# Optimization experiments

Measured on AMD Instinct MI355X. Metric: run time of the kernel, lower is better.

The kernel has to match this reference:

```python
import jax, jax.numpy as jnp
import numpy as np

D_MODEL = 1024
N_HEADS = 16
HEAD_DIM = D_MODEL // N_HEADS


def setup_inputs() -> dict:
    key = jax.random.key(0)
    ks = jax.random.split(key, 10)
    B, NQ, S = 8, 64, 4096
    inv = 1.0 / np.sqrt(D_MODEL)
    inp = {
        "queries": jax.random.normal(ks[0], (B, NQ, D_MODEL), dtype=jnp.float32),
        "context": jax.random.normal(ks[1], (B, S, D_MODEL), dtype=jnp.float32),
        "wq": jax.random.normal(ks[2], (D_MODEL, D_MODEL), dtype=jnp.float32) * inv,
        "bq": jnp.zeros((D_MODEL,), dtype=jnp.float32),
        "wk": jax.random.normal(ks[3], (D_MODEL, D_MODEL), dtype=jnp.float32) * inv,
        "bk": jnp.zeros((D_MODEL,), dtype=jnp.float32),
        "wv": jax.random.normal(ks[4], (D_MODEL, D_MODEL), dtype=jnp.float32) * inv,
        "bv": jnp.zeros((D_MODEL,), dtype=jnp.float32),
        "wo": jax.random.normal(ks[5], (D_MODEL, D_MODEL), dtype=jnp.float32) * inv,
        "bo": jnp.zeros((D_MODEL,), dtype=jnp.float32),
    }
    return inp


def reference(queries, context, wq, bq, wk, bk, wv, bv, wo, bo):
    B, NQ, D = queries.shape
    S = context.shape[1]
    H, HD = N_HEADS, HEAD_DIM
    scale = HD ** -0.5
    # projections (x @ W^T + b, matching nn.Linear)
    q = queries @ wq.T + bq            # (B, NQ, D)
    k = context @ wk.T + bk            # (B, S, D)
    v = context @ wv.T + bv            # (B, S, D)
    q = q.reshape(B, NQ, H, HD).transpose(0, 2, 1, 3)  # (B, H, NQ, HD)
    k = k.reshape(B, S, H, HD).transpose(0, 2, 1, 3)   # (B, H, S, HD)
    v = v.reshape(B, S, H, HD).transpose(0, 2, 1, 3)   # (B, H, S, HD)
    attn = jnp.einsum('bhnd,bhsd->bhns', q, k) * scale
    attn = jax.nn.softmax(attn, axis=-1)
    # dropout is identity at eval / p=0
    out = jnp.einsum('bhns,bhsd->bhnd', attn, v)        # (B, H, NQ, HD)
    out = out.transpose(0, 2, 1, 3).reshape(B, NQ, D)   # (B, NQ, D)
    return out @ wo.T + bo
```

## Files before the change

### kernel.cpp

```cpp
#include <hip/hip_runtime.h>
#include <stdint.h>

#define BATCH   8
#define NQL     64
#define SLEN    4096
#define DMODEL  1024
#define NHEADS  16
#define HDIM    64

typedef float          f32x4  __attribute__((ext_vector_type(4)));
typedef float          f32x16 __attribute__((ext_vector_type(16)));
typedef __bf16         bf16x8 __attribute__((ext_vector_type(8)));
typedef unsigned int   u32x4  __attribute__((ext_vector_type(4)));
typedef unsigned short u16x4  __attribute__((ext_vector_type(4)));
typedef unsigned short u16x8  __attribute__((ext_vector_type(8)));

__device__ __forceinline__ unsigned short f2bf(float f) {
  unsigned int u = __builtin_bit_cast(unsigned int, f);
  u += 0x7FFFu + ((u >> 16) & 1u);
  return (unsigned short)(u >> 16);
}

__device__ __forceinline__ f32x4 mfma16(bf16x8 a, bf16x8 b, f32x4 c) {
  return __builtin_amdgcn_mfma_f32_16x16x32_bf16(a, b, c, 0, 0, 0);
}

__device__ __forceinline__ bf16x8 lds_frag(const char* p) {
  u32x4 v = *(const u32x4*)p;
  return __builtin_bit_cast(bf16x8, v);
}

__device__ __forceinline__ void gload_lds16(const void* g, void* l) {
  __builtin_amdgcn_global_load_lds((const __attribute__((address_space(1))) void*)g,
                                   (__attribute__((address_space(3))) void*)l, 16, 0, 0);
}

__global__ __launch_bounds__(256) void cvt_bf16_kernel(const float* __restrict__ in,
                                                       unsigned short* __restrict__ out,
                                                       int n8) {
  int i = blockIdx.x * 256 + threadIdx.x;
  if (i >= n8) return;
  const float4* p = (const float4*)in + (size_t)i * 2;
  float4 a = p[0], b = p[1];
  u16x8 o;
  o[0] = f2bf(a.x); o[1] = f2bf(a.y); o[2] = f2bf(a.z); o[3] = f2bf(a.w);
  o[4] = f2bf(b.x); o[5] = f2bf(b.y); o[6] = f2bf(b.z); o[7] = f2bf(b.w);
  *((u16x8*)out + i) = o;
}

#define GF(a) ((a) ^ (((((a) >> 7) & 3) << 4) | ((((a) >> 9) & 1) << 6)))

template<int MODE>
__global__ __launch_bounds__(512, 2)
void gemm256(const unsigned short* __restrict__ A, const unsigned short* __restrict__ Bw,
             const float* __restrict__ bias, void* __restrict__ Cout,
             int M, int N, int K) {
  __shared__ char lds[98304];

  const int tid = threadIdx.x;
  const int wid = tid >> 6, lane = tid & 63;
  const int l31 = lane & 31, lhi = lane >> 5;
  const int wm = wid >> 2, wn = wid & 3;

  const int nbn = N >> 8;
  const int cpx = (int)gridDim.x >> 3;
  const int bid = (int)blockIdx.x;
  const int wg  = (bid & 7) * cpx + (bid >> 3);
  const int brow = (wg / nbn) << 8;
  const int bcol = (wg % nbn) << 8;

  const int dA0 = wid * 1024 + lane * 16;
  const int dA1 = dA0 + 8192;
  const int a0 = GF(dA0), a1 = GF(dA1);
  const int r0s = a0 >> 6, g0 = (a0 >> 4) & 3;
  const int r1s = a1 >> 6, g1 = (a1 >> 4) & 3;
  const unsigned short* srcA0 = A + (size_t)(brow + r0s) * K + g0 * 8;
  const unsigned short* srcA1 = A + (size_t)(brow + r1s) * K + g1 * 8;
  const unsigned short* srcB0 = Bw + (size_t)(bcol + r0s) * K + g0 * 8;
  const unsigned short* srcB1 = Bw + (size_t)(bcol + r1s) * K + g1 * 8;
  const int db0 = wid * 1024;
  const int db1 = db0 + 8192;

  int offA[4][2], offB[2][2];
#pragma unroll
  for (int mi = 0; mi < 4; ++mi)
#pragma unroll
    for (int ks = 0; ks < 2; ++ks) {
      int r = wm * 128 + mi * 32 + l31;
      int a = r * 64 + ks * 32 + lhi * 16;
      offA[mi][ks] = GF(a);
    }
#pragma unroll
  for (int ni = 0; ni < 2; ++ni)
#pragma unroll
    for (int ks = 0; ks < 2; ++ks) {
      int r = wn * 64 + ni * 32 + l31;
      int a = r * 64 + ks * 32 + lhi * 16;
      offB[ni][ks] = GF(a) + 16384;
    }

  f32x16 acc[4][2];
#pragma unroll
  for (int mi = 0; mi < 4; ++mi)
#pragma unroll
    for (int ni = 0; ni < 2; ++ni)
#pragma unroll
      for (int e = 0; e < 16; ++e) acc[mi][ni][e] = 0.f;

  auto stage = [&](int kt, int bo) {
    const int ko = kt << 5;
    char* base = lds + bo;
    gload_lds16(srcA0 + ko, base + db0);
    gload_lds16(srcA1 + ko, base + db1);
    gload_lds16(srcB0 + ko, base + 16384 + db0);
    gload_lds16(srcB1 + ko, base + 16384 + db1);
  };

  const int KT = K >> 5;
  stage(0, 0);
  stage(1, 32768);
  asm volatile("s_waitcnt vmcnt(4)" ::: "memory");
  __builtin_amdgcn_s_barrier();
  __builtin_amdgcn_sched_barrier(0);

  int bo = 0;
  for (int kt = 0; kt < KT; ++kt) {
    const bool st = (kt + 2 < KT);
    if (st) {
      int bo2 = bo + 65536;
      if (bo2 >= 98304) bo2 -= 98304;
      stage(kt + 2, bo2);
    }
    const char* bA = lds + bo;
    bf16x8 af[4][2], bfr[2][2];
#pragma unroll
    for (int mi = 0; mi < 4; ++mi)
#pragma unroll
      for (int ks = 0; ks < 2; ++ks) af[mi][ks] = lds_frag(bA + offA[mi][ks]);
#pragma unroll
    for (int ni = 0; ni < 2; ++ni)
#pragma unroll
      for (int ks = 0; ks < 2; ++ks) bfr[ni][ks] = lds_frag(bA + offB[ni][ks]);

    __builtin_amdgcn_s_setprio(1);
#pragma unroll
    for (int ks = 0; ks < 2; ++ks)
#pragma unroll
      for (int mi = 0; mi < 4; ++mi)
#pragma unroll
        for (int ni = 0; ni < 2; ++ni)
          acc[mi][ni] = __builtin_amdgcn_mfma_f32_32x32x16_bf16(af[mi][ks], bfr[ni][ks],
                                                                acc[mi][ni], 0, 0, 0);
    __builtin_amdgcn_s_setprio(0);

    if (kt + 1 < KT) {
      if (st) asm volatile("s_waitcnt vmcnt(4)" ::: "memory");
      else    asm volatile("s_waitcnt vmcnt(0)" ::: "memory");
      __builtin_amdgcn_s_barrier();
      __builtin_amdgcn_sched_barrier(0);
    }
    bo = (bo == 65536) ? 0 : bo + 32768;
  }

#pragma unroll
  for (int mi = 0; mi < 4; ++mi) {
#pragma unroll
    for (int ni = 0; ni < 2; ++ni) {
      f32x16 v = acc[mi][ni];
      const int c = bcol + wn * 64 + ni * 32 + l31;
      const float bi = bias[c];
      const int rbase = brow + wm * 128 + mi * 32 + lhi * 4;
      if constexpr (MODE == 0) {
        unsigned short* Cb = (unsigned short*)Cout;
#pragma unroll
        for (int q = 0; q < 4; ++q)
#pragma unroll
          for (int j = 0; j < 4; ++j)
            Cb[(size_t)(rbase + q * 8 + j) * N + c] = f2bf(v[q * 4 + j] + bi);
      } else {
        unsigned short* Vt = (unsigned short*)Cout;
        const size_t fb = ((size_t)(rbase >> 12) * 1024 + c) * 4096;
#pragma unroll
        for (int q = 0; q < 4; ++q) {
          u16x4 pk;
#pragma unroll
          for (int j = 0; j < 4; ++j) pk[j] = f2bf(v[q * 4 + j] + bi);
          *(u16x4*)(Vt + fb + ((rbase + q * 8) & 4095)) = pk;
        }
      }
    }
  }
}

template<int MODE>
__global__ __launch_bounds__(256)
void gemm_bt(const unsigned short* __restrict__ A, const unsigned short* __restrict__ Bw,
             const float* __restrict__ bias, void* __restrict__ Cout,
             int M, int N, int K) {
  __shared__ char lds[32768];
  char* ldsA = lds;
  char* ldsB = lds + 16384;

  const int tid  = threadIdx.x;
  const int wave = tid >> 6, lane = tid & 63;
  const int g    = lane >> 4, ln = lane & 15;
  const int nbn  = N >> 7;
  const int brow = (int)(blockIdx.x / nbn) << 7;
  const int bcol = (int)(blockIdx.x % nbn) << 7;
  const int wr   = wave >> 1, wc = wave & 1;

  f32x4 acc[4][4];
#pragma unroll
  for (int i = 0; i < 4; ++i)
#pragma unroll
    for (int j = 0; j < 4; ++j) acc[i][j] = (f32x4){0.f, 0.f, 0.f, 0.f};

  const int KT = K >> 6;
  const int srow = lane >> 3;
  const int srcs = (lane & 7) ^ (srow & 7);

  for (int kt = 0; kt < KT; ++kt) {
#pragma unroll
    for (int c = wave; c < 16; c += 4) {
      int row = (c << 3) + srow;
      const char* ga = (const char*)A + (((size_t)(brow + row) * K + (kt << 6) + (srcs << 3)) << 1);
      gload_lds16(ga, ldsA + (c << 10));
      const char* gb = (const char*)Bw + (((size_t)(bcol + row) * K + (kt << 6) + (srcs << 3)) << 1);
      gload_lds16(gb, ldsB + (c << 10));
    }
    asm volatile("s_waitcnt vmcnt(0)" ::: "memory");
    __syncthreads();

#pragma unroll
    for (int ks = 0; ks < 2; ++ks) {
      bf16x8 af[4], bfr[4];
      const int slot = ((ks << 2) + g) ^ (ln & 7);
#pragma unroll
      for (int mt = 0; mt < 4; ++mt) {
        int row = wr * 64 + mt * 16 + ln;
        af[mt] = lds_frag(ldsA + row * 128 + (slot << 4));
      }
#pragma unroll
      for (int nt = 0; nt < 4; ++nt) {
        int row = wc * 64 + nt * 16 + ln;
        bfr[nt] = lds_frag(ldsB + row * 128 + (slot << 4));
      }
      __builtin_amdgcn_s_setprio(1);
#pragma unroll
      for (int mt = 0; mt < 4; ++mt)
#pragma unroll
        for (int nt = 0; nt < 4; ++nt)
          acc[mt][nt] = mfma16(af[mt], bfr[nt], acc[mt][nt]);
      __builtin_amdgcn_s_setprio(0);
    }
    __syncthreads();
  }

#pragma unroll
  for (int mt = 0; mt < 4; ++mt) {
#pragma unroll
    for (int nt = 0; nt < 4; ++nt) {
      f32x4 v = acc[mt][nt];
      int r0 = brow + wr * 64 + mt * 16 + g * 4;
      int c  = bcol + wc * 64 + nt * 16 + ln;
      float bi = bias[c];
      if constexpr (MODE == 0) {
        unsigned short* Cb = (unsigned short*)Cout;
#pragma unroll
        for (int j = 0; j < 4; ++j) Cb[(size_t)(r0 + j) * N + c] = f2bf(v[j] + bi);
      } else {
        float* Cf = (float*)Cout;
#pragma unroll
        for (int j = 0; j < 4; ++j) Cf[(size_t)(r0 + j) * N + c] = v[j] + bi;
      }
    }
  }
}

__global__ __launch_bounds__(256)
void attn_kernel(const unsigned short* __restrict__ Qp,
                 const unsigned short* __restrict__ Kp,
                 const unsigned short* __restrict__ Vt,
                 unsigned short* __restrict__ Aout) {
  __shared__ char ldsKV[2][16384];
  __shared__ unsigned int plds[4 * 16 * 36];

  const int bh = blockIdx.x;
  const int b = bh >> 4, h = bh & 15;
  const int tid = threadIdx.x;
  const int wave = tid >> 6, lane = tid & 63;
  const int g = lane >> 4, ln = lane & 15;
  const int pbase = wave * 576 + ln * 36;
  const int srow = lane >> 3;
  const int srcs = (lane & 7) ^ (srow & 7);

  const unsigned short* qb =
      Qp + ((size_t)(b * 64 + wave * 16 + ln) * 1024) + h * 64 + g * 8;
  bf16x8 qf[2];
  qf[0] = __builtin_bit_cast(bf16x8, *(const u32x4*)qb);
  qf[1] = __builtin_bit_cast(bf16x8, *(const u32x4*)(qb + 32));

  f32x4 oacc[4];
#pragma unroll
  for (int i = 0; i < 4; ++i) oacc[i] = (f32x4){0.f, 0.f, 0.f, 0.f};
  float mrun = -1e30f, lrun = 0.f;

  auto stage = [&](int t, int buf) {
    int s0 = t << 6;
    char* bK = ldsKV[buf];
#pragma unroll
    for (int c4 = 0; c4 < 4; ++c4) {
      int c = wave * 4 + c4;
      int cc = c & 7;
      int row = (cc << 3) + srow;
      const char* gsrc;
      if (c < 8)
        gsrc = (const char*)Kp + (((size_t)((b << 12) + s0 + row) * 1024 + (h << 6) + (srcs << 3)) << 1);
      else
        gsrc = (const char*)Vt + (((size_t)((b << 10) + (h << 6) + row) * 4096 + s0 + (srcs << 3)) << 1);
      gload_lds16(gsrc, bK + ((c < 8) ? 0 : 8192) + (cc << 10));
    }
  };

  stage(0, 0);
  const int NT = SLEN / 64;
  for (int t = 0; t < NT; ++t) {
    asm volatile("s_waitcnt vmcnt(0)" ::: "memory");
    __syncthreads();
    if (t + 1 < NT) stage(t + 1, (t + 1) & 1);

    char* bufK = ldsKV[t & 1];
    char* bufV = bufK + 8192;

    f32x4 s4[4];
#pragma unroll
    for (int i = 0; i < 4; ++i) s4[i] = (f32x4){0.f, 0.f, 0.f, 0.f};
    __builtin_amdgcn_s_setprio(1);
#pragma unroll
    for (int ks = 0; ks < 2; ++ks) {
      const int slot = ((ks << 2) + g) ^ (ln & 7);
#pragma unroll
      for (int mt = 0; mt < 4; ++mt) {
        int row = mt * 16 + ln;
        s4[mt] = mfma16(lds_frag(bufK + row * 128 + (slot << 4)), qf[ks], s4[mt]);
      }
    }
    __builtin_amdgcn_s_setprio(0);

    float tmax = -1e30f;
#pragma unroll
    for (int mt = 0; mt < 4; ++mt)
#pragma unroll
      for (int j = 0; j < 4; ++j) {
        float sv = s4[mt][j] * 0.125f;
        s4[mt][j] = sv;
        tmax = fmaxf(tmax, sv);
      }
    tmax = fmaxf(tmax, __shfl_xor(tmax, 16));
    tmax = fmaxf(tmax, __shfl_xor(tmax, 32));
    float mnew = fmaxf(mrun, tmax);
    float factor = __expf(mrun - mnew);
    float psum = 0.f;
#pragma unroll
    for (int mt = 0; mt < 4; ++mt) {
      float p0 = __expf(s4[mt][0] - mnew);
      float p1 = __expf(s4[mt][1] - mnew);
      float p2 = __expf(s4[mt][2] - mnew);
      float p3 = __expf(s4[mt][3] - mnew);
      psum += (p0 + p1) + (p2 + p3);
      plds[pbase + mt * 8 + g * 2 + 0] = (unsigned)f2bf(p0) | ((unsigned)f2bf(p1) << 16);
      plds[pbase + mt * 8 + g * 2 + 1] = (unsigned)f2bf(p2) | ((unsigned)f2bf(p3) << 16);
    }
    psum += __shfl_xor(psum, 16);
    psum += __shfl_xor(psum, 32);
    lrun = lrun * factor + psum;
    mrun = mnew;

    float fj0 = __shfl(factor, g * 4 + 0);
    float fj1 = __shfl(factor, g * 4 + 1);
    float fj2 = __shfl(factor, g * 4 + 2);
    float fj3 = __shfl(factor, g * 4 + 3);
#pragma unroll
    for (int nt = 0; nt < 4; ++nt) {
      oacc[nt][0] *= fj0; oacc[nt][1] *= fj1; oacc[nt][2] *= fj2; oacc[nt][3] *= fj3;
    }

    __builtin_amdgcn_s_setprio(1);
#pragma unroll
    for (int kt2 = 0; kt2 < 2; ++kt2) {
      u32x4 pv;
      int pidx = pbase + kt2 * 16 + g * 4;
      pv[0] = plds[pidx]; pv[1] = plds[pidx + 1]; pv[2] = plds[pidx + 2]; pv[3] = plds[pidx + 3];
      bf16x8 pa = __builtin_bit_cast(bf16x8, pv);
      const int slot = ((kt2 << 2) + g) ^ (ln & 7);
#pragma unroll
      for (int nt = 0; nt < 4; ++nt) {
        int row = nt * 16 + ln;
        oacc[nt] = mfma16(pa, lds_frag(bufV + row * 128 + (slot << 4)), oacc[nt]);
      }
    }
    __builtin_amdgcn_s_setprio(0);
  }

  float l0 = __shfl(lrun, g * 4 + 0);
  float l1 = __shfl(lrun, g * 4 + 1);
  float l2 = __shfl(lrun, g * 4 + 2);
  float l3 = __shfl(lrun, g * 4 + 3);
  float r0 = 1.f / l0, r1 = 1.f / l1, r2 = 1.f / l2, r3 = 1.f / l3;
#pragma unroll
  for (int nt = 0; nt < 4; ++nt) {
    int col = h * 64 + nt * 16 + ln;
    size_t rbase = (size_t)(b * 64 + wave * 16 + g * 4) * 1024 + col;
    Aout[rbase + 0 * 1024] = f2bf(oacc[nt][0] * r0);
    Aout[rbase + 1 * 1024] = f2bf(oacc[nt][1] * r1);
    Aout[rbase + 2 * 1024] = f2bf(oacc[nt][2] * r2);
    Aout[rbase + 3 * 1024] = f2bf(oacc[nt][3] * r3);
  }
}

extern "C" void kernel_launch(void* const* d_in, const int* in_sizes, int n_in,
                              void* d_out, int out_size, void* d_ws, size_t ws_size,
                              hipStream_t stream) {
  const float* queries = (const float*)d_in[0];
  const float* context = (const float*)d_in[1];
  const float* wq = (const float*)d_in[2];
  const float* bq = (const float*)d_in[3];
  const float* wk = (const float*)d_in[4];
  const float* bk = (const float*)d_in[5];
  const float* wv = (const float*)d_in[6];
  const float* bv = (const float*)d_in[7];
  const float* wo = (const float*)d_in[8];
  const float* bo = (const float*)d_in[9];

  const size_t CTX_E = (size_t)BATCH * SLEN * DMODEL;
  const size_t QRY_E = (size_t)BATCH * NQL * DMODEL;
  const size_t W_E   = (size_t)DMODEL * DMODEL;

  char* ws = (char*)d_ws;
  size_t off = 0;
  auto alloc = [&](size_t bytes) {
    char* p = ws + off;
    off += (bytes + 255) & ~(size_t)255;
    return p;
  };
  unsigned short* ctx_bf = (unsigned short*)alloc(CTX_E * 2);
  unsigned short* q_bf   = (unsigned short*)alloc(QRY_E * 2);
  unsigned short* wq_bf  = (unsigned short*)alloc(W_E * 2);
  unsigned short* wk_bf  = (unsigned short*)alloc(W_E * 2);
  unsigned short* wv_bf  = (unsigned short*)alloc(W_E * 2);
  unsigned short* wo_bf  = (unsigned short*)alloc(W_E * 2);
  unsigned short* Qp     = (unsigned short*)alloc(QRY_E * 2);
  unsigned short* Kp     = (unsigned short*)alloc(CTX_E * 2);
  unsigned short* Vt     = (unsigned short*)alloc(CTX_E * 2);
  unsigned short* Ao     = (unsigned short*)alloc(QRY_E * 2);
  if (off > ws_size) return;

  cvt_bf16_kernel<<<dim3((int)(CTX_E / 8 / 256)), 256, 0, stream>>>(context, ctx_bf, (int)(CTX_E / 8));
  cvt_bf16_kernel<<<dim3((int)(QRY_E / 8 / 256)), 256, 0, stream>>>(queries, q_bf, (int)(QRY_E / 8));
  cvt_bf16_kernel<<<dim3((int)(W_E / 8 / 256)), 256, 0, stream>>>(wq, wq_bf, (int)(W_E / 8));
  cvt_bf16_kernel<<<dim3((int)(W_E / 8 / 256)), 256, 0, stream>>>(wk, wk_bf, (int)(W_E / 8));
  cvt_bf16_kernel<<<dim3((int)(W_E / 8 / 256)), 256, 0, stream>>>(wv, wv_bf, (int)(W_E / 8));
  cvt_bf16_kernel<<<dim3((int)(W_E / 8 / 256)), 256, 0, stream>>>(wo, wo_bf, (int)(W_E / 8));

  const int M_KV = BATCH * SLEN;
  const int M_Q  = BATCH * NQL;

  gemm256<0><<<dim3((M_KV / 256) * (DMODEL / 256)), 512, 0, stream>>>(ctx_bf, wk_bf, bk, Kp, M_KV, DMODEL, DMODEL);
  gemm256<2><<<dim3((M_KV / 256) * (DMODEL / 256)), 512, 0, stream>>>(ctx_bf, wv_bf, bv, Vt, M_KV, DMODEL, DMODEL);

  gemm_bt<0><<<dim3((M_Q / 128) * (DMODEL / 128)), 256, 0, stream>>>(q_bf, wq_bf, bq, Qp, M_Q, DMODEL, DMODEL);

  attn_kernel<<<dim3(BATCH * NHEADS), 256, 0, stream>>>(Qp, Kp, Vt, Ao);

  gemm_bt<1><<<dim3((M_Q / 128) * (DMODEL / 128)), 256, 0, stream>>>(Ao, wo_bf, bo, d_out, M_Q, DMODEL, DMODEL);
}
```

Before: 510.5 us.

## Split attention over sequence chunks with combine kernel; double-buffer gemm_bt

The attention kernel previously ran only 128 blocks (one per batch-head), each looping over all 4096 keys. This leaves most of the GPU's compute units idle. It now splits the sequence into 8 chunks, so 1024 blocks run. Each block writes partial output plus its running max and sum, and a new combine kernel merges them with log-sum-exp rescaling. The partial buffers reuse the ctx_bf workspace, which is dead by then. Separately, gemm_bt gets double-buffered LDS with async prefetch of the next K tile. This adds an extra launch and fp32 partial-result traffic.

```diff
diff --git a/kernel.cpp b/kernel.cpp
--- a/kernel.cpp
+++ b/kernel.cpp
@@ -7,6 +7,7 @@
 #define DMODEL  1024
 #define NHEADS  16
 #define HDIM    64
+#define NSPLIT  8
 
 typedef float          f32x4  __attribute__((ext_vector_type(4)));
 typedef float          f32x16 __attribute__((ext_vector_type(16)));
@@ -197,9 +198,7 @@
 void gemm_bt(const unsigned short* __restrict__ A, const unsigned short* __restrict__ Bw,
              const float* __restrict__ bias, void* __restrict__ Cout,
              int M, int N, int K) {
-  __shared__ char lds[32768];
-  char* ldsA = lds;
-  char* ldsB = lds + 16384;
+  __shared__ char lds[65536];
 
   const int tid  = threadIdx.x;
   const int wave = tid >> 6, lane = tid & 63;
@@ -219,17 +218,28 @@
   const int srow = lane >> 3;
   const int srcs = (lane & 7) ^ (srow & 7);
 
-  for (int kt = 0; kt < KT; ++kt) {
+  auto stage = [&](int kt, char* buf) {
 #pragma unroll
     for (int c = wave; c < 16; c += 4) {
       int row = (c << 3) + srow;
       const char* ga = (const char*)A + (((size_t)(brow + row) * K + (kt << 6) + (srcs << 3)) << 1);
-      gload_lds16(ga, ldsA + (c << 10));
+      gload_lds16(ga, buf + (c << 10));
       const char* gb = (const char*)Bw + (((size_t)(bcol + row) * K + (kt << 6) + (srcs << 3)) << 1);
-      gload_lds16(gb, ldsB + (c << 10));
-    }
-    asm volatile("s_waitcnt vmcnt(0)" ::: "memory");
-    __syncthreads();
+      gload_lds16(gb, buf + 16384 + (c << 10));
+    }
+  };
+
+  stage(0, lds);
+  for (int kt = 0; kt < KT; ++kt) {
+    char* cur = lds + ((kt & 1) << 15);
+    if (kt + 1 < KT) {
+      stage(kt + 1, lds + (((kt + 1) & 1) << 15));
+      asm volatile("s_waitcnt vmcnt(8)" ::: "memory");
+    } else {
+      asm volatile("s_waitcnt vmcnt(0)" ::: "memory");
+    }
+    __builtin_amdgcn_s_barrier();
+    __builtin_amdgcn_sched_barrier(0);
 
 #pragma unroll
     for (int ks = 0; ks < 2; ++ks) {
@@ -238,12 +248,12 @@
 #pragma unroll
       for (int mt = 0; mt < 4; ++mt) {
         int row = wr * 64 + mt * 16 + ln;
-        af[mt] = lds_frag(ldsA + row * 128 + (slot << 4));
+        af[mt] = lds_frag(cur + row * 128 + (slot << 4));
       }
 #pragma unroll
       for (int nt = 0; nt < 4; ++nt) {
         int row = wc * 64 + nt * 16 + ln;
-        bfr[nt] = lds_frag(ldsB + row * 128 + (slot << 4));
+        bfr[nt] = lds_frag(cur + 16384 + row * 128 + (slot << 4));
       }
       __builtin_amdgcn_s_setprio(1);
 #pragma unroll
@@ -253,7 +263,7 @@
           acc[mt][nt] = mfma16(af[mt], bfr[nt], acc[mt][nt]);
       __builtin_amdgcn_s_setprio(0);
     }
-    __syncthreads();
+    __builtin_amdgcn_s_barrier();
   }
 
 #pragma unroll
@@ -278,14 +288,17 @@
 }
 
 __global__ __launch_bounds__(256)
-void attn_kernel(const unsigned short* __restrict__ Qp,
-                 const unsigned short* __restrict__ Kp,
-                 const unsigned short* __restrict__ Vt,
-                 unsigned short* __restrict__ Aout) {
+void attn_split(const unsigned short* __restrict__ Qp,
+                const unsigned short* __restrict__ Kp,
+                const unsigned short* __restrict__ Vt,
+                float* __restrict__ Opart,
+                float* __restrict__ Mpart,
+                float* __restrict__ Lpart) {
   __shared__ char ldsKV[2][16384];
   __shared__ unsigned int plds[4 * 16 * 36];
 
-  const int bh = blockIdx.x;
+  const int bh = (int)blockIdx.x / NSPLIT;
+  const int sp = (int)blockIdx.x % NSPLIT;
   const int b = bh >> 4, h = bh & 15;
   const int tid = threadIdx.x;
   const int wave = tid >> 6, lane = tid & 63;
@@ -322,14 +335,15 @@
     }
   };
 
-  stage(0, 0);
-  const int NT = SLEN / 64;
-  for (int t = 0; t < NT; ++t) {
+  const int T0 = sp * (SLEN / 64 / NSPLIT);
+  const int NTL = SLEN / 64 / NSPLIT;
+  stage(T0, 0);
+  for (int tl = 0; tl < NTL; ++tl) {
     asm volatile("s_waitcnt vmcnt(0)" ::: "memory");
     __syncthreads();
-    if (t + 1 < NT) stage(t + 1, (t + 1) & 1);
-
-    char* bufK = ldsKV[t & 1];
+    if (tl + 1 < NTL) stage(T0 + tl + 1, (tl + 1) & 1);
+
+    char* bufK = ldsKV[tl & 1];
     char* bufV = bufK + 8192;
 
     f32x4 s4[4];
@@ -402,20 +416,46 @@
     __builtin_amdgcn_s_setprio(0);
   }
 
-  float l0 = __shfl(lrun, g * 4 + 0);
-  float l1 = __shfl(lrun, g * 4 + 1);
-  float l2 = __shfl(lrun, g * 4 + 2);
-  float l3 = __shfl(lrun, g * 4 + 3);
-  float r0 = 1.f / l0, r1 = 1.f / l1, r2 = 1.f / l2, r3 = 1.f / l3;
+  const int rowb = sp * (BATCH * NHEADS * 64) + bh * 64;
 #pragma unroll
   for (int nt = 0; nt < 4; ++nt) {
-    int col = h * 64 + nt * 16 + ln;
-    size_t rbase = (size_t)(b * 64 + wave * 16 + g * 4) * 1024 + col;
-    Aout[rbase + 0 * 1024] = f2bf(oacc[nt][0] * r0);
-    Aout[rbase + 1 * 1024] = f2bf(oacc[nt][1] * r1);
-    Aout[rbase + 2 * 1024] = f2bf(oacc[nt][2] * r2);
-    Aout[rbase + 3 * 1024] = f2bf(oacc[nt][3] * r3);
-  }
+#pragma unroll
+    for (int j = 0; j < 4; ++j) {
+      int q = wave * 16 + g * 4 + j;
+      Opart[(size_t)(rowb + q) * 64 + nt * 16 + ln] = oacc[nt][j];
+    }
+  }
+  if (g == 0) {
+    Mpart[rowb + wave * 16 + ln] = mrun;
+    Lpart[rowb + wave * 16 + ln] = lrun;
+  }
+}
+
+__global__ __launch_bounds__(256)
+void attn_combine(const float* __restrict__ Opart, const float* __restrict__ Mpart,
+                  const float* __restrict__ Lpart, unsigned short* __restrict__ Aout) {
+  const int blk = blockIdx.x;
+  const int bh = blk >> 4;
+  const int q  = ((blk & 15) << 2) + (threadIdx.x >> 6);
+  const int hd = threadIdx.x & 63;
+  const int row = bh * 64 + q;
+
+  float mi[NSPLIT];
+  float M = -1e30f;
+#pragma unroll
+  for (int i = 0; i < NSPLIT; ++i) {
+    mi[i] = Mpart[i * 8192 + row];
+    M = fmaxf(M, mi[i]);
+  }
+  float L = 0.f, o = 0.f;
+#pragma unroll
+  for (int i = 0; i < NSPLIT; ++i) {
+    float w = __expf(mi[i] - M);
+    L += Lpart[i * 8192 + row] * w;
+    o += Opart[(size_t)(i * 8192 + row) * 64 + hd] * w;
+  }
+  const int b = bh >> 4, h = bh & 15;
+  Aout[(size_t)(b * 64 + q) * 1024 + h * 64 + hd] = f2bf(o / L);
 }
 
 extern "C" void kernel_launch(void* const* d_in, const int* in_sizes, int n_in,
@@ -455,6 +495,10 @@
   unsigned short* Ao     = (unsigned short*)alloc(QRY_E * 2);
   if (off > ws_size) return;
 
+  float* Opart = (float*)ctx_bf;
+  float* Mpart = Opart + (size_t)NSPLIT * BATCH * NHEADS * 64 * 64;
+  float* Lpart = Mpart + (size_t)NSPLIT * BATCH * NHEADS * 64;
+
   cvt_bf16_kernel<<<dim3((int)(CTX_E / 8 / 256)), 256, 0, stream>>>(context, ctx_bf, (int)(CTX_E / 8));
   cvt_bf16_kernel<<<dim3((int)(QRY_E / 8 / 256)), 256, 0, stream>>>(queries, q_bf, (int)(QRY_E / 8));
   cvt_bf16_kernel<<<dim3((int)(W_E / 8 / 256)), 256, 0, stream>>>(wq, wq_bf, (int)(W_E / 8));
@@ -470,7 +514,8 @@
 
   gemm_bt<0><<<dim3((M_Q / 128) * (DMODEL / 128)), 256, 0, stream>>>(q_bf, wq_bf, bq, Qp, M_Q, DMODEL, DMODEL);
 
-  attn_kernel<<<dim3(BATCH * NHEADS), 256, 0, stream>>>(Qp, Kp, Vt, Ao);
+  attn_split<<<dim3(BATCH * NHEADS * NSPLIT), 256, 0, stream>>>(Qp, Kp, Vt, Opart, Mpart, Lpart);
+  attn_combine<<<dim3(BATCH * NHEADS * 16), 256, 0, stream>>>(Opart, Mpart, Lpart, Ao);
 
   gemm_bt<1><<<dim3((M_Q / 128) * (DMODEL / 128)), 256, 0, stream>>>(Ao, wo_bf, bo, d_out, M_Q, DMODEL, DMODEL);
 }
```

New measurement: 449.4 us. -12.0%, faster.
